# Performance work log

Hardware: AMD Instinct MI355X
Metric: run time of the kernel (lower is better)

The kernel has to match this reference:

```python
import jax, jax.numpy as jnp
import numpy as np

J = 25
C_IN, HID, LAT = 3, 64, 32


def _graph_conv(x, A, W, b):
    # x: [N,T,J,Cin]; A: [J,J]; W: [Cin,Cout]; b: [Cout]
    A = jax.nn.softmax(A, axis=-1)
    # fused adjacency mix + projection: (A @ x) @ W + b
    x = jnp.einsum('ij,ntjc->ntic', A, x)
    return jnp.einsum('ntjc,cd->ntjd', x, W) + b


def setup_inputs() -> dict:
    key = jax.random.key(0)
    ks = jax.random.split(key, 13)
    x = jax.random.normal(ks[0], (32, 2048, J, C_IN), dtype=jnp.float32)
    eye = jnp.eye(J, dtype=jnp.float32)
    def lin(kw, kb, cin, cout):
        W = jax.random.normal(kw, (cin, cout), dtype=jnp.float32) / np.sqrt(cin)
        b = jax.random.normal(kb, (cout,), dtype=jnp.float32) * 0.01
        return W, b
    W1, b1 = lin(ks[1], ks[2], C_IN, HID)
    W2, b2 = lin(ks[3], ks[4], HID, LAT)
    W3, b3 = lin(ks[5], ks[6], LAT, HID)
    W4, b4 = lin(ks[7], ks[8], HID, C_IN)
    return {
        'x': x,
        'A1': eye, 'W1': W1, 'b1': b1,
        'A2': eye, 'W2': W2, 'b2': b2,
        'A3': eye, 'W3': W3, 'b3': b3,
        'A4': eye, 'W4': W4, 'b4': b4,
    }


def reference(x, A1, W1, b1, A2, W2, b2, A3, W3, b3, A4, W4, b4):
    h = jax.nn.relu(_graph_conv(x, A1, W1, b1))     # encoder_g1 + relu
    z = _graph_conv(h, A2, W2, b2)                  # encoder_g2 (no relu)
    h_dec = jax.nn.relu(_graph_conv(z, A3, W3, b3)) # decoder_g1 + relu
    out = _graph_conv(h_dec, A4, W4, b4)            # decoder_g2
    return out
```

## Files before the change

### kernel.cpp

```cpp
#include <hip/hip_runtime.h>
#include <math.h>

#define J 25
#define NJC 75
#define NWAVE 4
#define NTHREADS 256
#define NFPW 32

#define O_A1P  0
#define O_APP  1024
#define O_A4B  2048
#define O_W2T  3072
#define O_W3T  5120
#define O_W1A  7168
#define O_W4C  8192
#define O_B4   8512
#define O_BPPF 8576
#define CWS_SZ 8704

using bf16x2 = __attribute__((ext_vector_type(2))) __bf16;
using bf16x8 = __attribute__((ext_vector_type(8))) __bf16;
using f32x4  = __attribute__((ext_vector_type(4))) float;
using f32x16 = __attribute__((ext_vector_type(16))) float;

__device__ inline bf16x8 zero8() {
    bf16x8 z;
    #pragma unroll
    for (int j = 0; j < 8; j++) z[j] = (__bf16)0.f;
    return z;
}

#if defined(__has_builtin)
#if __has_builtin(__builtin_amdgcn_cvt_pk_bf16_f32)
#define HAVE_PK_BF16 1
#endif
#endif

__device__ inline bf16x2 cvt2(float a, float b) {
#ifdef HAVE_PK_BF16
    return __builtin_amdgcn_cvt_pk_bf16_f32(a, b);
#else
    bf16x2 r; r[0] = (__bf16)a; r[1] = (__bf16)b; return r;
#endif
}
__device__ inline bf16x8 pk8(const f32x16& acc, int st) {
    const int b = 8 * st;
    bf16x8 r;
    #pragma unroll
    for (int p = 0; p < 4; p++) {
        bf16x2 v = cvt2(acc[b + 2 * p], acc[b + 2 * p + 1]);
        r[2 * p] = v[0]; r[2 * p + 1] = v[1];
    }
    return r;
}

__global__ __launch_bounds__(NTHREADS, 2) void gcn_fused(
    const float* __restrict__ x,
    const float* __restrict__ A1, const float* __restrict__ W1, const float* __restrict__ b1,
    const float* __restrict__ A2, const float* __restrict__ W2, const float* __restrict__ b2,
    const float* __restrict__ A3, const float* __restrict__ W3, const float* __restrict__ b3,
    const float* __restrict__ A4, const float* __restrict__ W4, const float* __restrict__ b4,
    float* __restrict__ out)
{
    __shared__ __align__(16) float  TS[3189];
    __shared__ __align__(16) __bf16 CWS[CWS_SZ];

    const int t = threadIdx.x;

    {
        float* T   = TS;
        float* bpp = T + 3125;
        float* T0 = T;        float* T1 = T + 625;  float* T2 = T + 1250;
        float* T3 = T + 1875; float* T4 = T + 2500;

        if (t < 100) {
            const int m = t / J, i = t % J;
            const float* Asrc = (m == 0) ? A1 : (m == 1) ? A2 : (m == 2) ? A3 : A4;
            float row[J];
            float mx = -1e30f;
            #pragma unroll
            for (int j = 0; j < J; j++) { row[j] = Asrc[i * J + j]; mx = fmaxf(mx, row[j]); }
            float s = 0.f;
            #pragma unroll
            for (int j = 0; j < J; j++) { row[j] = __expf(row[j] - mx); s += row[j]; }
            const float inv = 1.f / s;
            float* dst = T + m * 625 + i * J;
            #pragma unroll
            for (int j = 0; j < J; j++) dst[j] = row[j] * inv;
        }
        if (t < 64) {
            float s = b3[t];
            #pragma unroll
            for (int l = 0; l < 32; l++) s += W3[l * 64 + t] * b2[l];
            bpp[t] = s;
        }
        __syncthreads();

        for (int idx = t; idx < 625; idx += 256) {
            const int i = idx / J, jj = idx % J;
            float s = 0.f;
            #pragma unroll
            for (int k = 0; k < J; k++) s += T2[i * J + k] * T1[k * J + jj];
            T4[idx] = s;
        }
        __syncthreads();

        for (int i = t; i < 1024; i += 256) {
            const int b = i >> 8, n = (i >> 3) & 31, jj = i & 7;
            const int s = b >> 1, h = b & 1, r = 8 * s + jj;
            const int k32 = (r & 3) + 8 * (r >> 2) + 4 * h;
            const bool ok = (k32 < J && n < J);
            CWS[O_A1P + i] = (__bf16)(ok ? T0[n * J + k32] : 0.f);
            CWS[O_APP + i] = (__bf16)(ok ? T4[n * J + k32] : 0.f);
            CWS[O_A4B + i] = (__bf16)(ok ? T3[n * J + k32] : 0.f);
        }
        for (int i = t; i < 2048; i += 256) {
            {
                const int b = i >> 8, n = (i >> 3) & 31, jj = i & 7;
                const int s = b >> 1, h = b & 1, r = 8 * (s & 1) + jj;
                const int d = 32 * (s >> 1) + (r & 3) + 8 * (r >> 2) + 4 * h;
                CWS[O_W2T + i] = (__bf16)W2[d * 32 + n];
            }
            {
                const int tt = i >> 10, rr = i & 1023;
                const int b = rr >> 8, m = (rr >> 3) & 31, jj = rr & 7;
                const int s = b >> 1, h = b & 1, r = 8 * s + jj;
                const int l = (r & 3) + 8 * (r >> 2) + 4 * h;
                CWS[O_W3T + i] = (__bf16)W3[l * 64 + tt * 32 + m];
            }
        }
        for (int i = t; i < 1024; i += 256) {
            const int tile = i >> 9, rr = i & 511, hf_ = rr >> 8, n = (rr >> 3) & 31, jj = rr & 7;
            const int k = 8 * hf_ + jj;
            const int d = tile * 32 + n;
            float v = 0.f;
            if (k < 3) v = W1[k * 64 + d];
            else if (k == 3) v = b1[d];
            CWS[O_W1A + i] = (__bf16)v;
        }
        {
            const int c = t >> 6, b = (t >> 3) & 7, jj = t & 7;
            const int s = b >> 1, h = b & 1, r = 8 * (s & 1) + jj;
            const int d = 32 * (s >> 1) + (r & 3) + 8 * (r >> 2) + 4 * h;
            CWS[O_W4C + t] = (c < 3) ? (__bf16)W4[d * 3 + c] : (__bf16)0.f;
        }
        {
            float* fwB = (float*)(CWS + O_BPPF);
            if (t < 64) {
                const int g = t >> 4, h = (t >> 3) & 1, jj = t & 7;
                const int tt = g >> 1, st = g & 1;
                const int row32 = (jj & 3) + 16 * st + 8 * (jj >> 2) + 4 * h;
                fwB[t] = bpp[tt * 32 + row32];
            }
            float* fb4 = (float*)(CWS + O_B4);
            if (t >= 64 && t < 68) fb4[t - 64] = (t < 67) ? b4[t - 64] : 0.f;
        }
        __syncthreads();
    }

    const int w = t >> 6, lane = t & 63, ln = lane & 31, half = lane >> 5;
    const int fo = ln * 8;

    const long fbase = ((long)blockIdx.x * NWAVE + w) * NFPW;

    const float* xp = x + fbase * NJC;
    float* op = out + fbase * NJC;

    const bool xact = (lane < J);
    const int xoff = lane * 3;

    float xA0 = 0.f, xA1 = 0.f, xA2 = 0.f;
    float xB0 = 0.f, xB1 = 0.f, xB2 = 0.f;
    if (xact) {
        const float* q = xp + xoff;
        xA0 = q[0]; xA1 = q[1]; xA2 = q[2];
    }
    xp += NJC;
    if (xact) {
        const float* q = xp + xoff;
        xB0 = q[0]; xB1 = q[1]; xB2 = q[2];
    }
    xp += NJC;

    bf16x8 rA1P[2], rApp[2], rA4b[2], rW1A[2], rW2[4], rW3[4], rW4[4];
    #pragma unroll
    for (int ks = 0; ks < 2; ks++) {
        rA1P[ks] = *(const bf16x8*)&CWS[O_A1P + (2 * ks + half) * 256 + fo];
        rApp[ks] = *(const bf16x8*)&CWS[O_APP + (2 * ks + half) * 256 + fo];
        rA4b[ks] = *(const bf16x8*)&CWS[O_A4B + (2 * ks + half) * 256 + fo];
        rW1A[ks] = *(const bf16x8*)&CWS[O_W1A + ks * 512 + half * 256 + fo];
    }
    #pragma unroll
    for (int ks = 0; ks < 4; ks++)
        rW2[ks] = *(const bf16x8*)&CWS[O_W2T + (half + 2 * ks) * 256 + fo];
    #pragma unroll
    for (int tt = 0; tt < 2; tt++)
        #pragma unroll
        for (int ks = 0; ks < 2; ks++)
            rW3[tt * 2 + ks] = *(const bf16x8*)&CWS[O_W3T + tt * 1024 + (half + 2 * ks) * 256 + fo];
    #pragma unroll
    for (int ks = 0; ks < 4; ks++) {
        rW4[ks] = zero8();
        if (ln < 3) rW4[ks] = *(const bf16x8*)&CWS[O_W4C + ln * 64 + (half + 2 * ks) * 8];
    }
    f32x16 rB16[2];
    {
        const float* fwB = (const float*)(CWS + O_BPPF);
        #pragma unroll
        for (int tt = 0; tt < 2; tt++)
            #pragma unroll
            for (int st = 0; st < 2; st++) {
                f32x4 qa = *(const f32x4*)&fwB[32 * tt + 16 * st + 8 * half + 0];
                f32x4 qb = *(const f32x4*)&fwB[32 * tt + 16 * st + 8 * half + 4];
                #pragma unroll
                for (int j = 0; j < 4; j++) {
                    rB16[tt][8 * st + j]     = qa[j];
                    rB16[tt][8 * st + 4 + j] = qb[j];
                }
            }
    }
    const float* fb4 = (const float*)(CWS + O_B4);
    const float b40 = fb4[0], b41 = fb4[1], b42 = fb4[2];

    f32x16 Z;
    #pragma unroll
    for (int z = 0; z < 16; z++) Z[z] = 0.f;

    const bool do_store = (lane < J);

    auto frame = [&](bf16x8 xa, float* opp) {
        f32x16 accG0 = __builtin_amdgcn_mfma_f32_32x32x16_bf16(xa, rW1A[0], Z, 0, 0, 0);
        f32x16 accG1 = __builtin_amdgcn_mfma_f32_32x32x16_bf16(xa, rW1A[1], Z, 0, 0, 0);
        bf16x8 ga0 = pk8(accG0, 0), ga1 = pk8(accG0, 1);
        bf16x8 ga2 = pk8(accG1, 0), ga3 = pk8(accG1, 1);

        bf16x8 hf[4];
        {
            f32x16 accH0 = __builtin_amdgcn_mfma_f32_32x32x16_bf16(ga0, rA1P[0], Z, 0, 0, 0);
            accH0 = __builtin_amdgcn_mfma_f32_32x32x16_bf16(ga1, rA1P[1], accH0, 0, 0, 0);
            f32x16 accH1 = __builtin_amdgcn_mfma_f32_32x32x16_bf16(ga2, rA1P[0], Z, 0, 0, 0);
            accH1 = __builtin_amdgcn_mfma_f32_32x32x16_bf16(ga3, rA1P[1], accH1, 0, 0, 0);
            #pragma unroll
            for (int z = 0; z < 16; z++) {
                accH0[z] = fmaxf(accH0[z], 0.f);
                accH1[z] = fmaxf(accH1[z], 0.f);
            }
            hf[0] = pk8(accH0, 0); hf[1] = pk8(accH0, 1);
            hf[2] = pk8(accH1, 0); hf[3] = pk8(accH1, 1);
        }

        f32x16 accU = __builtin_amdgcn_mfma_f32_32x32x16_bf16(hf[0], rW2[0], Z, 0, 0, 0);
        #pragma unroll
        for (int s = 1; s < 4; s++)
            accU = __builtin_amdgcn_mfma_f32_32x32x16_bf16(hf[s], rW2[s], accU, 0, 0, 0);
        bf16x8 uf[2] = { pk8(accU, 0), pk8(accU, 1) };

        f32x16 accV = __builtin_amdgcn_mfma_f32_32x32x16_bf16(uf[0], rApp[0], Z, 0, 0, 0);
        accV = __builtin_amdgcn_mfma_f32_32x32x16_bf16(uf[1], rApp[1], accV, 0, 0, 0);
        bf16x8 vf[2] = { pk8(accV, 0), pk8(accV, 1) };

        bf16x8 hd[4];
        #pragma unroll
        for (int tt = 0; tt < 2; tt++) {
            f32x16 acc = __builtin_amdgcn_mfma_f32_32x32x16_bf16(rW3[tt * 2 + 0], vf[0], rB16[tt], 0, 0, 0);
            acc = __builtin_amdgcn_mfma_f32_32x32x16_bf16(rW3[tt * 2 + 1], vf[1], acc, 0, 0, 0);
            #pragma unroll
            for (int z = 0; z < 16; z++) acc[z] = fmaxf(acc[z], 0.f);
            hd[2 * tt]     = pk8(acc, 0);
            hd[2 * tt + 1] = pk8(acc, 1);
        }

        f32x16 accP = __builtin_amdgcn_mfma_f32_32x32x16_bf16(hd[0], rW4[0], Z, 0, 0, 0);
        #pragma unroll
        for (int s = 1; s < 4; s++)
            accP = __builtin_amdgcn_mfma_f32_32x32x16_bf16(hd[s], rW4[s], accP, 0, 0, 0);
        bf16x8 pf[2] = { pk8(accP, 0), pk8(accP, 1) };

        f32x16 accO = __builtin_amdgcn_mfma_f32_32x32x16_bf16(pf[0], rA4b[0], Z, 0, 0, 0);
        accO = __builtin_amdgcn_mfma_f32_32x32x16_bf16(pf[1], rA4b[1], accO, 0, 0, 0);
        if (do_store) {
            opp[lane * 3 + 0] = accO[0] + b40;
            opp[lane * 3 + 1] = accO[1] + b41;
            opp[lane * 3 + 2] = accO[2] + b42;
        }
    };

    #pragma unroll 1
    for (int fi = 0; fi < NFPW; fi += 2) {
        bf16x8 xaA = zero8();
        if (xact) {
            xaA[0] = (__bf16)xA0; xaA[1] = (__bf16)xA1;
            xaA[2] = (__bf16)xA2; xaA[3] = (__bf16)1.f;
        }
        if (fi + 2 < NFPW) {
            if (xact) {
                const float* q = xp + xoff;
                xA0 = q[0]; xA1 = q[1]; xA2 = q[2];
            }
        }
        xp += NJC;
        frame(xaA, op);
        op += NJC;

        bf16x8 xaB = zero8();
        if (xact) {
            xaB[0] = (__bf16)xB0; xaB[1] = (__bf16)xB1;
            xaB[2] = (__bf16)xB2; xaB[3] = (__bf16)1.f;
        }
        if (fi + 3 < NFPW) {
            if (xact) {
                const float* q = xp + xoff;
                xB0 = q[0]; xB1 = q[1]; xB2 = q[2];
            }
        }
        xp += NJC;
        frame(xaB, op);
        op += NJC;
    }
}

extern "C" void kernel_launch(void* const* d_in, const int* in_sizes, int n_in,
                              void* d_out, int out_size, void* d_ws, size_t ws_size,
                              hipStream_t stream)
{
    const float* x  = (const float*)d_in[0];
    const float* A1 = (const float*)d_in[1];
    const float* W1 = (const float*)d_in[2];
    const float* b1 = (const float*)d_in[3];
    const float* A2 = (const float*)d_in[4];
    const float* W2 = (const float*)d_in[5];
    const float* b2 = (const float*)d_in[6];
    const float* A3 = (const float*)d_in[7];
    const float* W3 = (const float*)d_in[8];
    const float* b3 = (const float*)d_in[9];
    const float* A4 = (const float*)d_in[10];
    const float* W4 = (const float*)d_in[11];
    const float* b4 = (const float*)d_in[12];
    float* out = (float*)d_out;
    (void)d_ws; (void)ws_size;

    const int NT = in_sizes[0] / NJC;
    const int nblocks = NT / (NWAVE * NFPW);

    gcn_fused<<<nblocks, NTHREADS, 0, stream>>>(
        x, A1, W1, b1, A2, W2, b2, A3, W3, b3, A4, W4, b4, out);
}
```

Measured before the change: 136.5 us.

## Switch to persistent grid-stride frame pairs with three blocks per CU

```diff
diff --git a/kernel.cpp b/kernel.cpp
--- a/kernel.cpp
+++ b/kernel.cpp
@@ -5,7 +5,9 @@
 #define NJC 75
 #define NWAVE 4
 #define NTHREADS 256
-#define NFPW 32
+#define NBLOCKS 768
+#define NPAIRS 32768
+#define WSTRIDE (NBLOCKS * NWAVE)
 
 #define O_A1P  0
 #define O_APP  1024
@@ -54,7 +56,7 @@
     return r;
 }
 
-__global__ __launch_bounds__(NTHREADS, 2) void gcn_fused(
+__global__ __launch_bounds__(NTHREADS, 3) void gcn_fused(
     const float* __restrict__ x,
     const float* __restrict__ A1, const float* __restrict__ W1, const float* __restrict__ b1,
     const float* __restrict__ A2, const float* __restrict__ W2, const float* __restrict__ b2,
@@ -161,10 +163,7 @@
     const int w = t >> 6, lane = t & 63, ln = lane & 31, half = lane >> 5;
     const int fo = ln * 8;
 
-    const long fbase = ((long)blockIdx.x * NWAVE + w) * NFPW;
-
-    const float* xp = x + fbase * NJC;
-    float* op = out + fbase * NJC;
+    const int wid = blockIdx.x * NWAVE + w;
 
     const bool xact = (lane < J);
     const int xoff = lane * 3;
@@ -172,15 +171,10 @@
     float xA0 = 0.f, xA1 = 0.f, xA2 = 0.f;
     float xB0 = 0.f, xB1 = 0.f, xB2 = 0.f;
     if (xact) {
-        const float* q = xp + xoff;
+        const float* q = x + (long)(2 * wid) * NJC + xoff;
         xA0 = q[0]; xA1 = q[1]; xA2 = q[2];
-    }
-    xp += NJC;
-    if (xact) {
-        const float* q = xp + xoff;
-        xB0 = q[0]; xB1 = q[1]; xB2 = q[2];
-    }
-    xp += NJC;
+        xB0 = q[NJC + 0]; xB1 = q[NJC + 1]; xB2 = q[NJC + 2];
+    }
 
     bf16x8 rA1P[2], rApp[2], rA4b[2], rW1A[2], rW2[4], rW3[4], rW4[4];
     #pragma unroll
@@ -286,36 +280,25 @@
     };
 
     #pragma unroll 1
-    for (int fi = 0; fi < NFPW; fi += 2) {
-        bf16x8 xaA = zero8();
+    for (long pair = wid; pair < NPAIRS; pair += WSTRIDE) {
+        float* opp = out + (2 * pair) * NJC;
+
+        bf16x8 xaA = zero8(), xaB = zero8();
         if (xact) {
             xaA[0] = (__bf16)xA0; xaA[1] = (__bf16)xA1;
             xaA[2] = (__bf16)xA2; xaA[3] = (__bf16)1.f;
-        }
-        if (fi + 2 < NFPW) {
-            if (xact) {
-                const float* q = xp + xoff;
-                xA0 = q[0]; xA1 = q[1]; xA2 = q[2];
-            }
-        }
-        xp += NJC;
-        frame(xaA, op);
-        op += NJC;
-
-        bf16x8 xaB = zero8();
-        if (xact) {
             xaB[0] = (__bf16)xB0; xaB[1] = (__bf16)xB1;
             xaB[2] = (__bf16)xB2; xaB[3] = (__bf16)1.f;
         }
-        if (fi + 3 < NFPW) {
-            if (xact) {
-                const float* q = xp + xoff;
-                xB0 = q[0]; xB1 = q[1]; xB2 = q[2];
-            }
-        }
-        xp += NJC;
-        frame(xaB, op);
-        op += NJC;
+        const long npair = pair + WSTRIDE;
+        if (npair < NPAIRS && xact) {
+            const float* q = x + (2 * npair) * NJC + xoff;
+            xA0 = q[0]; xA1 = q[1]; xA2 = q[2];
+            xB0 = q[NJC + 0]; xB1 = q[NJC + 1]; xB2 = q[NJC + 2];
+        }
+
+        frame(xaA, opp);
+        frame(xaB, opp + NJC);
     }
 }
 
@@ -339,9 +322,6 @@
     float* out = (float*)d_out;
     (void)d_ws; (void)ws_size;
 
-    const int NT = in_sizes[0] / NJC;
-    const int nblocks = NT / (NWAVE * NFPW);
-
-    gcn_fused<<<nblocks, NTHREADS, 0, stream>>>(
+    gcn_fused<<<NBLOCKS, NTHREADS, 0, stream>>>(
         x, A1, W1, b1, A2, W2, b2, A3, W3, b3, A4, W4, b4, out);
 }
```

Measured after the change: 139.2 us. Within noise of the previous version (+2.0%).

## Fold W2·W3 into one 64x64 weight and reorder the adjacency mixes

Applied to the files above, without the earlier changes.

```diff
diff --git a/kernel.cpp b/kernel.cpp
--- a/kernel.cpp
+++ b/kernel.cpp
@@ -10,8 +10,7 @@
 #define O_A1P  0
 #define O_APP  1024
 #define O_A4B  2048
-#define O_W2T  3072
-#define O_W3T  5120
+#define O_W23  3072
 #define O_W1A  7168
 #define O_W4C  8192
 #define O_B4   8512
@@ -62,7 +61,7 @@
     const float* __restrict__ A4, const float* __restrict__ W4, const float* __restrict__ b4,
     float* __restrict__ out)
 {
-    __shared__ __align__(16) float  TS[3189];
+    __shared__ __align__(16) float  TS[4096];
     __shared__ __align__(16) __bf16 CWS[CWS_SZ];
 
     const int t = threadIdx.x;
@@ -113,21 +112,6 @@
             CWS[O_A1P + i] = (__bf16)(ok ? T0[n * J + k32] : 0.f);
             CWS[O_APP + i] = (__bf16)(ok ? T4[n * J + k32] : 0.f);
             CWS[O_A4B + i] = (__bf16)(ok ? T3[n * J + k32] : 0.f);
-        }
-        for (int i = t; i < 2048; i += 256) {
-            {
-                const int b = i >> 8, n = (i >> 3) & 31, jj = i & 7;
-                const int s = b >> 1, h = b & 1, r = 8 * (s & 1) + jj;
-                const int d = 32 * (s >> 1) + (r & 3) + 8 * (r >> 2) + 4 * h;
-                CWS[O_W2T + i] = (__bf16)W2[d * 32 + n];
-            }
-            {
-                const int tt = i >> 10, rr = i & 1023;
-                const int b = rr >> 8, m = (rr >> 3) & 31, jj = rr & 7;
-                const int s = b >> 1, h = b & 1, r = 8 * s + jj;
-                const int l = (r & 3) + 8 * (r >> 2) + 4 * h;
-                CWS[O_W3T + i] = (__bf16)W3[l * 64 + tt * 32 + m];
-            }
         }
         for (int i = t; i < 1024; i += 256) {
             const int tile = i >> 9, rr = i & 511, hf_ = rr >> 8, n = (rr >> 3) & 31, jj = rr & 7;
@@ -156,6 +140,24 @@
             if (t >= 64 && t < 68) fb4[t - 64] = (t < 67) ? b4[t - 64] : 0.f;
         }
         __syncthreads();
+
+        for (int idx = t; idx < 4096; idx += 256) {
+            const int d = idx >> 6, dp = idx & 63;
+            float s = 0.f;
+            #pragma unroll
+            for (int l = 0; l < 32; l++) s += W2[d * 32 + l] * W3[l * 64 + dp];
+            TS[idx] = s;
+        }
+        __syncthreads();
+
+        for (int i = t; i < 4096; i += 256) {
+            const int tile = i >> 11, rr = i & 2047;
+            const int b = rr >> 8, n = (rr >> 3) & 31, jj = rr & 7;
+            const int s = b >> 1, h = b & 1, r = 8 * (s & 1) + jj;
+            const int d = 32 * (s >> 1) + (r & 3) + 8 * (r >> 2) + 4 * h;
+            CWS[O_W23 + i] = (__bf16)TS[d * 64 + tile * 32 + n];
+        }
+        __syncthreads();
     }
 
     const int w = t >> 6, lane = t & 63, ln = lane & 31, half = lane >> 5;
@@ -174,15 +176,11 @@
     if (xact) {
         const float* q = xp + xoff;
         xA0 = q[0]; xA1 = q[1]; xA2 = q[2];
-    }
-    xp += NJC;
-    if (xact) {
-        const float* q = xp + xoff;
-        xB0 = q[0]; xB1 = q[1]; xB2 = q[2];
-    }
-    xp += NJC;
-
-    bf16x8 rA1P[2], rApp[2], rA4b[2], rW1A[2], rW2[4], rW3[4], rW4[4];
+        xB0 = q[NJC + 0]; xB1 = q[NJC + 1]; xB2 = q[NJC + 2];
+    }
+    xp += 2 * NJC;
+
+    bf16x8 rA1P[2], rApp[2], rA4b[2], rW1A[2], rW23[8], rW4[4];
     #pragma unroll
     for (int ks = 0; ks < 2; ks++) {
         rA1P[ks] = *(const bf16x8*)&CWS[O_A1P + (2 * ks + half) * 256 + fo];
@@ -191,13 +189,11 @@
         rW1A[ks] = *(const bf16x8*)&CWS[O_W1A + ks * 512 + half * 256 + fo];
     }
     #pragma unroll
-    for (int ks = 0; ks < 4; ks++)
-        rW2[ks] = *(const bf16x8*)&CWS[O_W2T + (half + 2 * ks) * 256 + fo];
-    #pragma unroll
-    for (int tt = 0; tt < 2; tt++)
+    for (int tile = 0; tile < 2; tile++)
         #pragma unroll
-        for (int ks = 0; ks < 2; ks++)
-            rW3[tt * 2 + ks] = *(const bf16x8*)&CWS[O_W3T + tt * 1024 + (half + 2 * ks) * 256 + fo];
+        for (int ks = 0; ks < 4; ks++)
+            rW23[tile * 4 + ks] =
+                *(const bf16x8*)&CWS[O_W23 + tile * 2048 + (half + 2 * ks) * 256 + fo];
     #pragma unroll
     for (int ks = 0; ks < 4; ks++) {
         rW4[ks] = zero8();
@@ -249,25 +245,29 @@
             hf[2] = pk8(accH1, 0); hf[3] = pk8(accH1, 1);
         }
 
-        f32x16 accU = __builtin_amdgcn_mfma_f32_32x32x16_bf16(hf[0], rW2[0], Z, 0, 0, 0);
+        f32x16 accU0 = __builtin_amdgcn_mfma_f32_32x32x16_bf16(hf[0], rW23[0], Z, 0, 0, 0);
+        f32x16 accU1 = __builtin_amdgcn_mfma_f32_32x32x16_bf16(hf[0], rW23[4], Z, 0, 0, 0);
         #pragma unroll
-        for (int s = 1; s < 4; s++)
-            accU = __builtin_amdgcn_mfma_f32_32x32x16_bf16(hf[s], rW2[s], accU, 0, 0, 0);
-        bf16x8 uf[2] = { pk8(accU, 0), pk8(accU, 1) };
-
-        f32x16 accV = __builtin_amdgcn_mfma_f32_32x32x16_bf16(uf[0], rApp[0], Z, 0, 0, 0);
-        accV = __builtin_amdgcn_mfma_f32_32x32x16_bf16(uf[1], rApp[1], accV, 0, 0, 0);
-        bf16x8 vf[2] = { pk8(accV, 0), pk8(accV, 1) };
+        for (int s = 1; s < 4; s++) {
+            accU0 = __builtin_amdgcn_mfma_f32_32x32x16_bf16(hf[s], rW23[s], accU0, 0, 0, 0);
+            accU1 = __builtin_amdgcn_mfma_f32_32x32x16_bf16(hf[s], rW23[4 + s], accU1, 0, 0, 0);
+        }
+        bf16x8 uw0 = pk8(accU0, 0), uw1 = pk8(accU0, 1);
+        bf16x8 uw2 = pk8(accU1, 0), uw3 = pk8(accU1, 1);
 
         bf16x8 hd[4];
-        #pragma unroll
-        for (int tt = 0; tt < 2; tt++) {
-            f32x16 acc = __builtin_amdgcn_mfma_f32_32x32x16_bf16(rW3[tt * 2 + 0], vf[0], rB16[tt], 0, 0, 0);
-            acc = __builtin_amdgcn_mfma_f32_32x32x16_bf16(rW3[tt * 2 + 1], vf[1], acc, 0, 0, 0);
-            #pragma unroll
-            for (int z = 0; z < 16; z++) acc[z] = fmaxf(acc[z], 0.f);
-            hd[2 * tt]     = pk8(acc, 0);
-            hd[2 * tt + 1] = pk8(acc, 1);
+        {
+            f32x16 a0 = __builtin_amdgcn_mfma_f32_32x32x16_bf16(uw0, rApp[0], rB16[0], 0, 0, 0);
+            a0 = __builtin_amdgcn_mfma_f32_32x32x16_bf16(uw1, rApp[1], a0, 0, 0, 0);
+            f32x16 a1 = __builtin_amdgcn_mfma_f32_32x32x16_bf16(uw2, rApp[0], rB16[1], 0, 0, 0);
+            a1 = __builtin_amdgcn_mfma_f32_32x32x16_bf16(uw3, rApp[1], a1, 0, 0, 0);
+            #pragma unroll
+            for (int z = 0; z < 16; z++) {
+                a0[z] = fmaxf(a0[z], 0.f);
+                a1[z] = fmaxf(a1[z], 0.f);
+            }
+            hd[0] = pk8(a0, 0); hd[1] = pk8(a0, 1);
+            hd[2] = pk8(a1, 0); hd[3] = pk8(a1, 1);
         }
 
         f32x16 accP = __builtin_amdgcn_mfma_f32_32x32x16_bf16(hd[0], rW4[0], Z, 0, 0, 0);
@@ -292,30 +292,21 @@
             xaA[0] = (__bf16)xA0; xaA[1] = (__bf16)xA1;
             xaA[2] = (__bf16)xA2; xaA[3] = (__bf16)1.f;
         }
-        if (fi + 2 < NFPW) {
-            if (xact) {
-                const float* q = xp + xoff;
-                xA0 = q[0]; xA1 = q[1]; xA2 = q[2];
-            }
-        }
-        xp += NJC;
-        frame(xaA, op);
-        op += NJC;
-
         bf16x8 xaB = zero8();
         if (xact) {
             xaB[0] = (__bf16)xB0; xaB[1] = (__bf16)xB1;
             xaB[2] = (__bf16)xB2; xaB[3] = (__bf16)1.f;
         }
-        if (fi + 3 < NFPW) {
-            if (xact) {
-                const float* q = xp + xoff;
-                xB0 = q[0]; xB1 = q[1]; xB2 = q[2];
-            }
-        }
-        xp += NJC;
-        frame(xaB, op);
-        op += NJC;
+        if (fi + 2 < NFPW && xact) {
+            const float* q = xp + xoff;
+            xA0 = q[0]; xA1 = q[1]; xA2 = q[2];
+            xB0 = q[NJC + 0]; xB1 = q[NJC + 1]; xB2 = q[NJC + 2];
+        }
+        xp += 2 * NJC;
+
+        frame(xaA, op);
+        frame(xaB, op + NJC);
+        op += 2 * NJC;
     }
 }
 
```

Result: slower. 141.3 us (+3.6%).
